# Performance work log

Hardware: AMD Instinct MI355X
Metric: run time of the kernel (lower is better)

The kernel has to match this reference:

```python
import jax, jax.numpy as jnp
import numpy as np

B, T, I, H, O = 64, 1024, 512, 768, 512


def setup_inputs() -> dict:
    key = jax.random.key(0)
    ks = jax.random.split(key, 8)
    x_seq = jax.random.normal(ks[0], (B, T, I), dtype=jnp.float32)
    s = 0.02
    # Gate order along the 4H axis: f, i, g, o (matches the torch module's gates).
    Wx_f = jax.random.normal(ks[1], (4 * H, I), dtype=jnp.float32) * s
    Wh_f = jax.random.normal(ks[2], (4 * H, H), dtype=jnp.float32) * s
    Wx_b = jax.random.normal(ks[3], (4 * H, I), dtype=jnp.float32) * s
    Wh_b = jax.random.normal(ks[4], (4 * H, H), dtype=jnp.float32) * s
    # forget-gate bias init to 1.0 (f_Wxf.bias / b_Wxf.bias), rest 0
    b_gate = jnp.concatenate([jnp.ones((H,), jnp.float32), jnp.zeros((3 * H,), jnp.float32)])
    b_f = b_gate
    b_b = b_gate
    Why = jax.random.normal(ks[5], (O, 2 * H), dtype=jnp.float32) * s
    by = jnp.zeros((O,), jnp.float32)
    return {"x_seq": x_seq, "Wx_f": Wx_f, "Wh_f": Wh_f, "b_f": b_f,
            "Wx_b": Wx_b, "Wh_b": Wh_b, "b_b": b_b, "Why": Why, "by": by}


def _lstm_dir(x, Wx, Wh, b):
    # Precompute all input-to-gate projections in one fused GEMM over time.
    xp = jnp.einsum('bti,gi->btg', x, Wx) + b  # (B, T, 4H)

    def step(carry, xp_t):
        h, c = carry
        z = xp_t + h @ Wh.T                     # (B, 4H)
        f = jax.nn.sigmoid(z[:, 0 * H:1 * H])
        i = jax.nn.sigmoid(z[:, 1 * H:2 * H])
        g = jnp.tanh(z[:, 2 * H:3 * H])
        o = jax.nn.sigmoid(z[:, 3 * H:4 * H])
        c = f * c + i * g
        h = o * jnp.tanh(c)
        return (h, c), None

    h0 = jnp.zeros((x.shape[0], H), x.dtype)
    c0 = jnp.zeros((x.shape[0], H), x.dtype)
    (h, c), _ = jax.lax.scan(step, (h0, c0), jnp.swapaxes(xp, 0, 1))
    return h, c


def reference(x_seq, Wx_f, Wh_f, b_f, Wx_b, Wh_b, b_b, Why, by):
    h_fwd, c_fwd = _lstm_dir(x_seq, Wx_f, Wh_f, b_f)
    h_bwd, c_bwd = _lstm_dir(x_seq[:, ::-1, :], Wx_b, Wh_b, b_b)
    h_combined = jnp.concatenate([h_fwd, h_bwd], axis=1)  # (B, 2H)
    out = h_combined @ Why.T + by
    return out, h_fwd, c_fwd, h_bwd, c_bwd
```

## Files before the change

kernel.cpp:

```cpp
#include <hip/hip_runtime.h>
#include <hip/hip_cooperative_groups.h>

namespace cg = cooperative_groups;

#define B_ 64
#define T_ 1024
#define I_ 512
#define H_ 768
#define O_ 512
#define G4 3072
#define JB 16
#define NJ 48
#define NWGS 192

typedef short short8 __attribute__((ext_vector_type(8)));
typedef float f32x4 __attribute__((ext_vector_type(4)));
typedef int int4v __attribute__((ext_vector_type(4)));
typedef unsigned long long u64;

#define XBF_BYTES  (67108864)
#define WCAT_BYTES (15728640)
#define HBUF_BYTES (393216)

__device__ __forceinline__ unsigned short f32_to_bf16(float f) {
    union { float f; unsigned int u; } v; v.f = f;
    unsigned int r = v.u + 0x7fffu + ((v.u >> 16) & 1u);
    return (unsigned short)(r >> 16);
}
__device__ __forceinline__ float sigmoid_f(float x) { return 1.0f / (1.0f + __expf(-x)); }
__device__ __forceinline__ float tanh_f(float x) {
    float e = __expf(2.0f * x);
    return 1.0f - 2.0f / (e + 1.0f);
}

__device__ __forceinline__ void glds16(const void* g, void* l) {
    __builtin_amdgcn_global_load_lds(
        (const __attribute__((address_space(1))) unsigned int*)g,
        (__attribute__((address_space(3))) unsigned int*)l, 16, 0, 0);
}

__device__ __forceinline__ void ldsbar() {
    asm volatile("s_waitcnt lgkmcnt(0)" ::: "memory");
    __builtin_amdgcn_sched_barrier(0);
    __builtin_amdgcn_s_barrier();
    __builtin_amdgcn_sched_barrier(0);
}

__global__ void prep_x_kernel(const float* __restrict__ x, unsigned short* __restrict__ xb) {
    const size_t n = (size_t)B_ * T_ * 64;
    for (size_t i = (size_t)blockIdx.x * blockDim.x + threadIdx.x; i < n;
         i += (size_t)gridDim.x * blockDim.x) {
        int b  = (int)(i >> 16);
        int t  = (int)((i >> 6) & 1023);
        int kb = (int)(i & 63);
        const float4 v0 = *(const float4*)(x + i * 8);
        const float4 v1 = *(const float4*)(x + i * 8 + 4);
        short8 o;
        o[0] = (short)f32_to_bf16(v0.x); o[1] = (short)f32_to_bf16(v0.y);
        o[2] = (short)f32_to_bf16(v0.z); o[3] = (short)f32_to_bf16(v0.w);
        o[4] = (short)f32_to_bf16(v1.x); o[5] = (short)f32_to_bf16(v1.y);
        o[6] = (short)f32_to_bf16(v1.z); o[7] = (short)f32_to_bf16(v1.w);
        *(short8*)(xb + (((size_t)t * 64 + kb) * 64 + b) * 8) = o;
    }
}

__global__ void prep_w_kernel(const float* __restrict__ Wx_f, const float* __restrict__ Wh_f,
                              const float* __restrict__ Wx_b, const float* __restrict__ Wh_b,
                              unsigned short* __restrict__ w2, unsigned short* __restrict__ h2,
                              unsigned* __restrict__ bar) {
    const size_t n = (size_t)2 * G4 * 160;
    for (size_t i = (size_t)blockIdx.x * blockDim.x + threadIdx.x; i < n;
         i += (size_t)gridDim.x * blockDim.x) {
        int dir = (int)(i / 491520);
        int r2  = (int)(i % 491520);
        int row = r2 / 160;
        int kb  = r2 % 160;
        const float* Wx = dir ? Wx_b : Wx_f;
        const float* Wh = dir ? Wh_b : Wh_f;
        const float* src = (kb < 64) ? (Wx + (size_t)row * I_ + kb * 8)
                                     : (Wh + (size_t)row * H_ + (kb - 64) * 8);
        const float4 v0 = *(const float4*)(src);
        const float4 v1 = *(const float4*)(src + 4);
        short8 o;
        o[0] = (short)f32_to_bf16(v0.x); o[1] = (short)f32_to_bf16(v0.y);
        o[2] = (short)f32_to_bf16(v0.z); o[3] = (short)f32_to_bf16(v0.w);
        o[4] = (short)f32_to_bf16(v1.x); o[5] = (short)f32_to_bf16(v1.y);
        o[6] = (short)f32_to_bf16(v1.z); o[7] = (short)f32_to_bf16(v1.w);
        *(short8*)(w2 + (((size_t)dir * 160 + kb) * G4 + row) * 8) = o;
        if (i < 24576) {
            short8 z = {0,0,0,0,0,0,0,0};
            *(short8*)(h2 + i * 8) = z;
        }
        if (i < 512) bar[i] = 0u;
    }
}

__global__ void __launch_bounds__(512, 2)
bilstm_kernel(const float* __restrict__ bias_f, const float* __restrict__ bias_b,
              const unsigned short* __restrict__ xb, const unsigned short* __restrict__ w2,
              unsigned short* h2, unsigned* bar, float* d_out) {
    __shared__ unsigned short x_lds[64 * 32 * 8];
    __shared__ unsigned short h_lds[96 * 32 * 8];
    __shared__ float z_lds[4][32][17];
    __shared__ float c_tile[32][16];

    const int tid   = threadIdx.x;
    const int wg    = blockIdx.x;
    const int dir   = wg / 96;
    const int rem   = wg % 96;
    const int bh    = rem / NJ;
    const int jb    = rem % NJ;
    const int j0    = jb * JB;
    const int wave  = tid >> 6;
    const int lane  = tid & 63;
    const int gate  = wave & 3;
    const int mhalf = wave >> 2;
    const int quad  = lane >> 4;
    const int lrow  = lane & 15;
    const int m0l   = mhalf * 16 + lrow;

    c_tile[tid >> 4][tid & 15] = 0.0f;

    const float bias_r = (dir ? bias_b : bias_f)[gate * H_ + j0 + lrow];
    const int wrow = gate * H_ + j0 + lrow;

    const unsigned short* wx = w2 + (((size_t)dir * 160 + quad) * G4 + wrow) * 8;
    short8 wh[24];
#pragma unroll
    for (int ks = 0; ks < 24; ++ks)
        wh[ks] = *(const short8*)(w2 + (((size_t)dir * 160 + 64 + ks * 4 + quad) * G4 + wrow) * 8);

    const int group = dir * 2 + bh;
    unsigned* mybar = bar + (group * 4 + (jb & 3)) * 32;
    unsigned* barbase = bar + group * 4 * 32;

    const int src_off = (tid >> 5) * 1024 + bh * 512 + (tid & 31) * 16;

    char* const lds_wb   = (char*)x_lds + wave * 1024;
    char* const lds_mine = (char*)h_lds + tid * 16;
    const unsigned short* vax = x_lds + quad * 256 + m0l * 8;
    const unsigned short* vah = h_lds + quad * 256 + m0l * 8;

    {
        const int tx0 = dir ? (T_ - 1) : 0;
        const char* xsrc = (const char*)(xb + (size_t)tx0 * 32768) + src_off;
#pragma unroll
        for (int k = 0; k < 4; ++k) glds16(xsrc + k * 16384, lds_wb + k * 8192);
    }
    __syncthreads();

    for (int t = 0; t < T_; ++t) {
        const int pb = (t + 1) & 1;
        const int cb = t & 1;

        f32x4 acc0; acc0[0] = bias_r; acc0[1] = bias_r; acc0[2] = bias_r; acc0[3] = bias_r;

#pragma unroll
        for (int ks = 0; ks < 16; ++ks) {
            short8 a0 = *(const short8*)(vax + ks * 1024);
            short8 bf = *(const short8*)(wx + (size_t)ks * 4 * G4 * 8);
            acc0 = __builtin_amdgcn_mfma_f32_16x16x32_bf16(a0, bf, acc0, 0, 0, 0);
        }

        if (tid == 0) {
            const unsigned tgt = (unsigned)(NJ * t);
            for (;;) {
                unsigned ssum = 0;
#pragma unroll
                for (int i = 0; i < 4; ++i)
                    ssum += __hip_atomic_load(barbase + i * 32, __ATOMIC_RELAXED,
                                              __HIP_MEMORY_SCOPE_AGENT);
                if (ssum >= tgt) break;
                __builtin_amdgcn_s_sleep(1);
            }
        }
        asm volatile("" ::: "memory");
        __syncthreads();

        {
            const char* hp = (const char*)(h2 + (size_t)(dir * 2 + pb) * 49152) + src_off;
            int4v u0, u1, u2, u3, u4, u5;
#define HL(n) asm volatile("global_load_dwordx4 %0, %1, off sc1" : "=v"(u##n) : "v"(hp + (n) * 16384))
#define HS(n) *(int4v*)(lds_mine + (n) * 8192) = u##n
            HL(0); HL(1); HL(2); HL(3); HL(4); HL(5);
            asm volatile("s_waitcnt vmcnt(5)" ::: "memory"); HS(0);
            asm volatile("s_waitcnt vmcnt(4)" ::: "memory"); HS(1);
            asm volatile("s_waitcnt vmcnt(3)" ::: "memory"); HS(2);
            asm volatile("s_waitcnt vmcnt(2)" ::: "memory"); HS(3);
            asm volatile("s_waitcnt vmcnt(1)" ::: "memory"); HS(4);
            asm volatile("s_waitcnt vmcnt(0)" ::: "memory"); HS(5);
#undef HL
#undef HS
        }

        if (t + 1 < T_) {
            const int tx2 = dir ? (T_ - 2 - t) : (t + 1);
            const char* xsrc = (const char*)(xb + (size_t)tx2 * 32768) + src_off;
#pragma unroll
            for (int k = 0; k < 4; ++k) glds16(xsrc + k * 16384, lds_wb + k * 8192);
        }
        ldsbar();

#pragma unroll
        for (int ks = 0; ks < 24; ++ks) {
            short8 a0 = *(const short8*)(vah + ks * 1024);
            acc0 = __builtin_amdgcn_mfma_f32_16x16x32_bf16(a0, wh[ks], acc0, 0, 0, 0);
        }

#pragma unroll
        for (int r = 0; r < 4; ++r)
            z_lds[gate][mhalf * 16 + quad * 4 + r][lrow] = acc0[r];
        ldsbar();

        {
            unsigned short* hw = h2 + (size_t)(dir * 2 + cb) * 49152;
            const int gb  = tid >> 4;
            const int gj  = tid & 15;
            const int gjj = j0 + gj;
            const int bg  = bh * 32 + gb;
            float f0 = sigmoid_f(z_lds[0][gb][gj]);
            float i0 = sigmoid_f(z_lds[1][gb][gj]);
            float g0 = tanh_f(z_lds[2][gb][gj]);
            float o0 = sigmoid_f(z_lds[3][gb][gj]);
            float c0 = f0 * c_tile[gb][gj] + i0 * g0;
            c_tile[gb][gj] = c0;
            float h0 = o0 * tanh_f(c0);
            unsigned hv = (unsigned)f32_to_bf16(h0);
            unsigned ov = __shfl_xor(hv, 1);
            if (!(gj & 1)) {
                unsigned pack = hv | (ov << 16);
                unsigned* dst = (unsigned*)(hw + ((gjj >> 3) * 64 + bg) * 8 + (gjj & 7));
                __hip_atomic_store(dst, pack, __ATOMIC_RELAXED, __HIP_MEMORY_SCOPE_AGENT);
            }
            if (t == T_ - 1) {
                int hoff = 32768 + dir * 98304;
                d_out[hoff + bg * H_ + gjj]         = h0;
                d_out[hoff + 49152 + bg * H_ + gjj] = c0;
            }
        }
        __syncthreads();

        if (tid == 0)
            __hip_atomic_fetch_add(mybar, 1u, __ATOMIC_RELAXED, __HIP_MEMORY_SCOPE_AGENT);
    }
}

__global__ void proj_kernel(float* __restrict__ out, const float* __restrict__ Why,
                            const float* __restrict__ by) {
    __shared__ float hc[2 * H_];
    int b = blockIdx.x;
    const float* hf = out + 32768 + b * H_;
    const float* hb = out + 32768 + 98304 + b * H_;
    for (int i = threadIdx.x; i < H_; i += 256) { hc[i] = hf[i]; hc[H_ + i] = hb[i]; }
    __syncthreads();
    for (int o = threadIdx.x; o < O_; o += 256) {
        const float* wr = Why + (size_t)o * (2 * H_);
        float s = by[o];
        for (int k = 0; k < 2 * H_; k += 4) {
            float4 w = *(const float4*)(wr + k);
            s += w.x * hc[k] + w.y * hc[k + 1] + w.z * hc[k + 2] + w.w * hc[k + 3];
        }
        out[b * O_ + o] = s;
    }
}

extern "C" void kernel_launch(void* const* d_in, const int* in_sizes, int n_in,
                              void* d_out, int out_size, void* d_ws, size_t ws_size,
                              hipStream_t stream) {
    const float* x    = (const float*)d_in[0];
    const float* Wx_f = (const float*)d_in[1];
    const float* Wh_f = (const float*)d_in[2];
    const float* b_f  = (const float*)d_in[3];
    const float* Wx_b = (const float*)d_in[4];
    const float* Wh_b = (const float*)d_in[5];
    const float* b_b  = (const float*)d_in[6];
    const float* Why  = (const float*)d_in[7];
    const float* by   = (const float*)d_in[8];
    float* out = (float*)d_out;

    char* ws = (char*)d_ws;
    unsigned short* xbp = (unsigned short*)(ws);
    unsigned short* w2  = (unsigned short*)(ws + XBF_BYTES);
    unsigned short* h2  = (unsigned short*)(ws + XBF_BYTES + WCAT_BYTES);
    unsigned*       bar = (unsigned*)(ws + XBF_BYTES + WCAT_BYTES + HBUF_BYTES);

    prep_x_kernel<<<8192, 256, 0, stream>>>(x, xbp);
    prep_w_kernel<<<4096, 256, 0, stream>>>(Wx_f, Wh_f, Wx_b, Wh_b, w2, h2, bar);

    void* args[] = {(void*)&b_f, (void*)&b_b, (void*)&xbp, (void*)&w2,
                    (void*)&h2, (void*)&bar, (void*)&out};
    hipLaunchCooperativeKernel((void*)bilstm_kernel, dim3(NWGS), dim3(512), args, 0, stream);

    proj_kernel<<<B_, 256, 0, stream>>>(out, Why, by);
}
```

Baseline: 3.024 ms.

## Pipeline h-state chunk loads with recurrent MFMAs and split accumulator chains

The recurrent h-state fetch is split into six chunks. Each chunk is written to LDS and consumed by its slice of MFMAs as soon as it arrives, so compute overlaps the remaining global loads instead of waiting for all of them. MFMA accumulation is also split across two independent accumulators, shortening the dependent chain, and they are summed before the gate store. This adds five extra LDS barriers per timestep, which could offset the gain on this latency-bound serial loop.

```diff
diff --git a/kernel.cpp b/kernel.cpp
--- a/kernel.cpp
+++ b/kernel.cpp
@@ -16,7 +16,6 @@
 typedef short short8 __attribute__((ext_vector_type(8)));
 typedef float f32x4 __attribute__((ext_vector_type(4)));
 typedef int int4v __attribute__((ext_vector_type(4)));
-typedef unsigned long long u64;
 
 #define XBF_BYTES  (67108864)
 #define WCAT_BYTES (15728640)
@@ -154,12 +153,14 @@
         const int cb = t & 1;
 
         f32x4 acc0; acc0[0] = bias_r; acc0[1] = bias_r; acc0[2] = bias_r; acc0[3] = bias_r;
+        f32x4 acc1; acc1[0] = 0.f; acc1[1] = 0.f; acc1[2] = 0.f; acc1[3] = 0.f;
 
 #pragma unroll
         for (int ks = 0; ks < 16; ++ks) {
             short8 a0 = *(const short8*)(vax + ks * 1024);
             short8 bf = *(const short8*)(wx + (size_t)ks * 4 * G4 * 8);
-            acc0 = __builtin_amdgcn_mfma_f32_16x16x32_bf16(a0, bf, acc0, 0, 0, 0);
+            if (ks & 1) acc1 = __builtin_amdgcn_mfma_f32_16x16x32_bf16(a0, bf, acc1, 0, 0, 0);
+            else        acc0 = __builtin_amdgcn_mfma_f32_16x16x32_bf16(a0, bf, acc0, 0, 0, 0);
         }
 
         if (tid == 0) {
@@ -177,22 +178,33 @@
         asm volatile("" ::: "memory");
         __syncthreads();
 
-        {
-            const char* hp = (const char*)(h2 + (size_t)(dir * 2 + pb) * 49152) + src_off;
-            int4v u0, u1, u2, u3, u4, u5;
+        const char* hp = (const char*)(h2 + (size_t)(dir * 2 + pb) * 49152) + src_off;
+        int4v u0, u1, u2, u3, u4, u5;
 #define HL(n) asm volatile("global_load_dwordx4 %0, %1, off sc1" : "=v"(u##n) : "v"(hp + (n) * 16384))
-#define HS(n) *(int4v*)(lds_mine + (n) * 8192) = u##n
-            HL(0); HL(1); HL(2); HL(3); HL(4); HL(5);
-            asm volatile("s_waitcnt vmcnt(5)" ::: "memory"); HS(0);
-            asm volatile("s_waitcnt vmcnt(4)" ::: "memory"); HS(1);
-            asm volatile("s_waitcnt vmcnt(3)" ::: "memory"); HS(2);
-            asm volatile("s_waitcnt vmcnt(2)" ::: "memory"); HS(3);
-            asm volatile("s_waitcnt vmcnt(1)" ::: "memory"); HS(4);
-            asm volatile("s_waitcnt vmcnt(0)" ::: "memory"); HS(5);
+        HL(0); HL(1); HL(2); HL(3); HL(4); HL(5);
 #undef HL
-#undef HS
-        }
-
+        __builtin_amdgcn_sched_barrier(0);
+
+#define CHUNK(c, uc, CNT)                                                        \
+        asm volatile("s_waitcnt vmcnt(" CNT ")" ::: "memory");                   \
+        *(int4v*)(lds_mine + (c) * 8192) = uc;                                   \
+        ldsbar();                                                                \
+        _Pragma("unroll")                                                        \
+        for (int ks = 4 * (c); ks < 4 * (c) + 4; ++ks) {                         \
+            short8 a0 = *(const short8*)(vah + ks * 1024);                       \
+            if (ks & 1) acc1 = __builtin_amdgcn_mfma_f32_16x16x32_bf16(a0, wh[ks], acc1, 0, 0, 0); \
+            else        acc0 = __builtin_amdgcn_mfma_f32_16x16x32_bf16(a0, wh[ks], acc0, 0, 0, 0); \
+        }                                                                        \
+        __builtin_amdgcn_sched_barrier(0);
+
+        CHUNK(0, u0, "5")
+        CHUNK(1, u1, "4")
+        CHUNK(2, u2, "3")
+        CHUNK(3, u3, "2")
+        CHUNK(4, u4, "1")
+
+        asm volatile("s_waitcnt vmcnt(0)" ::: "memory");
+        *(int4v*)(lds_mine + 5 * 8192) = u5;
         if (t + 1 < T_) {
             const int tx2 = dir ? (T_ - 2 - t) : (t + 1);
             const char* xsrc = (const char*)(xb + (size_t)tx2 * 32768) + src_off;
@@ -200,16 +212,19 @@
             for (int k = 0; k < 4; ++k) glds16(xsrc + k * 16384, lds_wb + k * 8192);
         }
         ldsbar();
-
-#pragma unroll
-        for (int ks = 0; ks < 24; ++ks) {
+#pragma unroll
+        for (int ks = 20; ks < 24; ++ks) {
             short8 a0 = *(const short8*)(vah + ks * 1024);
-            acc0 = __builtin_amdgcn_mfma_f32_16x16x32_bf16(a0, wh[ks], acc0, 0, 0, 0);
-        }
+            if (ks & 1) acc1 = __builtin_amdgcn_mfma_f32_16x16x32_bf16(a0, wh[ks], acc1, 0, 0, 0);
+            else        acc0 = __builtin_amdgcn_mfma_f32_16x16x32_bf16(a0, wh[ks], acc0, 0, 0, 0);
+        }
+#undef CHUNK
+
+        f32x4 zv = acc0 + acc1;
 
 #pragma unroll
         for (int r = 0; r < 4; ++r)
-            z_lds[gate][mhalf * 16 + quad * 4 + r][lrow] = acc0[r];
+            z_lds[gate][mhalf * 16 + quad * 4 + r][lrow] = zv[r];
         ldsbar();
 
         {
```

Result: slower. 3.359 ms (+11.1%).
